# Performance work log

Measured on AMD Instinct MI355X. Metric: run time of the kernel, lower is better.

The kernel has to match this reference:

```python
import jax, jax.numpy as jnp
import numpy as np

D_MODEL = 1024
N_HEADS = 16
D_HEAD = D_MODEL // N_HEADS
BLOCK = 2048
EPS = 1e-5


def layer_norm(x, w, b):
    mu = jnp.mean(x, axis=-1, keepdims=True)
    var = jnp.mean(jnp.square(x - mu), axis=-1, keepdims=True)
    return (x - mu) * jax.lax.rsqrt(var + EPS) * w + b


def setup_inputs() -> dict:
    key = jax.random.key(0)
    ks = jax.random.split(key, 8)
    d = D_MODEL
    s = 1.0 / np.sqrt(d)
    return {
        "x": jax.random.normal(ks[0], (2, 2048, d), dtype=jnp.float32),
        "ln1_w": jnp.ones((d,), jnp.float32),
        "ln1_b": jnp.zeros((d,), jnp.float32),
        "ln2_w": jnp.ones((d,), jnp.float32),
        "ln2_b": jnp.zeros((d,), jnp.float32),
        "qkv_w": jax.random.normal(ks[1], (3 * d, d), jnp.float32) * s,
        "o_w": jax.random.normal(ks[2], (d, d), jnp.float32) * s,
        "ffn_w1": jax.random.normal(ks[3], (4 * d, d), jnp.float32) * s,
        "ffn_b1": jnp.zeros((4 * d,), jnp.float32),
        "ffn_w2": jax.random.normal(ks[4], (d, 4 * d), jnp.float32) * (1.0 / np.sqrt(4 * d)),
        "ffn_b2": jnp.zeros((d,), jnp.float32),
    }


def reference(x, ln1_w, ln1_b, ln2_w, ln2_b, qkv_w, o_w, ffn_w1, ffn_b1, ffn_w2, ffn_b2):
    b, n, d = x.shape
    h = layer_norm(x, ln1_w, ln1_b)
    # qkv: (b, n, 3, H, Dh)
    qkv = (h @ qkv_w.T).reshape(b, n, 3, N_HEADS, D_HEAD)
    q, k, v = qkv[:, :, 0], qkv[:, :, 1], qkv[:, :, 2]  # (b, n, H, Dh)
    scale = 1.0 / np.sqrt(D_HEAD)
    s = jnp.einsum("bqhd,bkhd->bhqk", q, k) * scale
    mask = jnp.tril(jnp.ones((n, n), dtype=bool))
    s = jnp.where(mask, s, -jnp.inf)
    a = jax.nn.softmax(s, axis=-1)
    attn_out = jnp.einsum("bhqk,bkhd->bqhd", a, v).reshape(b, n, d)
    x = x + attn_out @ o_w.T
    h2 = layer_norm(x, ln2_w, ln2_b)
    ff = jax.nn.gelu(h2 @ ffn_w1.T + ffn_b1, approximate=False) @ ffn_w2.T + ffn_b2
    return x + ff
```

## Files before the change

kernel.cpp:

```cpp
#include <hip/hip_runtime.h>
#include <math.h>

#define D_MODEL 1024
#define N_HEADS 16
#define D_HEAD  64
#define SEQ     2048
#define BATCH   2
#define M_TOT   (BATCH*SEQ)
#define FFN_DIM 4096

typedef __attribute__((ext_vector_type(8))) short bf16x8;
typedef __attribute__((ext_vector_type(4))) float f32x4;
typedef __attribute__((ext_vector_type(8))) unsigned short u16x8;

__device__ __forceinline__ unsigned short f2bf(float f) {
  unsigned int u = __float_as_uint(f);
  return (unsigned short)((u + 0x7fffu + ((u >> 16) & 1u)) >> 16);
}
__device__ __forceinline__ unsigned short f2bf_trunc(float f) {
  return (unsigned short)(__float_as_uint(f) >> 16);
}
__device__ __forceinline__ float bf2f(unsigned short s) {
  return __uint_as_float(((unsigned int)s) << 16);
}

__device__ __forceinline__ float gelu_exact(float x) {
  return 0.5f * x * (1.f + erff(x * 0.70710678118654752f));
}

__global__ __launch_bounds__(256) void cvt_all(const float* __restrict__ qkv_w,
    const float* __restrict__ o_w, const float* __restrict__ w1,
    const float* __restrict__ w2, unsigned short* __restrict__ dst) {
  const long MEGc = 1024*1024;
  long i = (long)(blockIdx.x*256 + threadIdx.x)*4;
  const float* src; long off;
  if (i < 3*MEGc)      { src = qkv_w; off = i; }
  else if (i < 4*MEGc) { src = o_w;  off = i - 3*MEGc; }
  else if (i < 8*MEGc) { src = w1;   off = i - 4*MEGc; }
  else                 { src = w2;   off = i - 8*MEGc; }
  float4 v = *(const float4*)(src + off);
  ushort4 o = { f2bf(v.x), f2bf(v.y), f2bf(v.z), f2bf(v.w) };
  *(ushort4*)(dst + i) = o;
}

__global__ __launch_bounds__(256) void ln_kernel(const float* __restrict__ x,
    const float* __restrict__ w, const float* __restrict__ b,
    unsigned short* __restrict__ out) {
  int row = blockIdx.x;
  const float* xr = x + (size_t)row * D_MODEL;
  int c = threadIdx.x * 4;
  float4 v = *(const float4*)(xr + c);
  float s = v.x + v.y + v.z + v.w;
  __shared__ float red[4];
  #pragma unroll
  for (int o = 32; o > 0; o >>= 1) s += __shfl_down(s, o, 64);
  int wave = threadIdx.x >> 6;
  if ((threadIdx.x & 63) == 0) red[wave] = s;
  __syncthreads();
  float mean = (red[0]+red[1]+red[2]+red[3]) * (1.f/D_MODEL);
  __syncthreads();
  float d0 = v.x-mean, d1 = v.y-mean, d2 = v.z-mean, d3 = v.w-mean;
  float s2 = d0*d0 + d1*d1 + d2*d2 + d3*d3;
  #pragma unroll
  for (int o = 32; o > 0; o >>= 1) s2 += __shfl_down(s2, o, 64);
  if ((threadIdx.x & 63) == 0) red[wave] = s2;
  __syncthreads();
  float var = (red[0]+red[1]+red[2]+red[3]) * (1.f/D_MODEL);
  float rs = rsqrtf(var + 1e-5f);
  float4 wv = *(const float4*)(w + c);
  float4 bv = *(const float4*)(b + c);
  ushort4 o = { f2bf(d0*rs*wv.x + bv.x), f2bf(d1*rs*wv.y + bv.y),
                f2bf(d2*rs*wv.z + bv.z), f2bf(d3*rs*wv.w + bv.w) };
  *(ushort4*)(out + (size_t)row*D_MODEL + c) = o;
}

__device__ __forceinline__ void swizzle_block(int nbx, int nby, int& bx, int& by) {
  int nb = nbx * nby;
  int bid = blockIdx.y * nbx + blockIdx.x;
  int chunk = nb >> 3;
  int bid2 = (bid & 7) * chunk + (bid >> 3);
  const int GM = 8;
  int ngroup = GM * nbx;
  int g = bid2 / ngroup, rem = bid2 % ngroup;
  by = g*GM + (rem % GM);
  bx = rem / GM;
}

template<int EPI, bool OBF, int BN>
__global__ __launch_bounds__(256) void gemm_mfma(
    const unsigned short* __restrict__ A, const unsigned short* __restrict__ Bt,
    float* __restrict__ Cf, unsigned short* __restrict__ Cb,
    const float* __restrict__ bias, const float* __restrict__ res,
    int M, int N, int K) {
  constexpr int BM = 128, BK = 32;
  constexpr int TS = (BM + BN) * BK;
  constexpr int CPT = TS / 2048;
  constexpr int NI = (BN == 128) ? 4 : 2;
  __shared__ unsigned short Ls[2][TS];
  int tid = threadIdx.x;
  int w = tid >> 6, l = tid & 63;
  int lg = l >> 4, lm = l & 15;
  int bx, by;
  swizzle_block(N/BN, M/BM, bx, by);
  int bm = by * BM, bn = bx * BN;
  int wm = (w >> 1) * 64;
  int wn = (w & 1) * (BN/2);

  f32x4 acc[4][NI];
  #pragma unroll
  for (int i = 0; i < 4; ++i)
    #pragma unroll
    for (int j = 0; j < NI; ++j)
      acc[i][j] = (f32x4){0.f, 0.f, 0.f, 0.f};

  const unsigned short* gp[CPT];
  int lo[CPT];
  #pragma unroll
  for (int i = 0; i < CPT; ++i) {
    int fc = i*256 + tid;
    int r = fc >> 2;
    int swz = (fc >> 3) & 3;
    int col = ((fc & 3) ^ swz) * 8;
    lo[i] = fc * 8;
    gp[i] = (r < BM) ? (A  + (size_t)(bm + r)*K + col)
                     : (Bt + (size_t)(bn + (r - BM))*K + col);
  }
  u16x8 sreg[CPT];
  auto loadregs = [&](int k0) {
    #pragma unroll
    for (int i = 0; i < CPT; ++i) sreg[i] = *(const u16x8*)(gp[i] + k0);
  };
  auto dswrite = [&](int buf) {
    #pragma unroll
    for (int i = 0; i < CPT; ++i) *(u16x8*)&Ls[buf][lo[i]] = sreg[i];
  };

  int lgs = lg ^ ((lm >> 1) & 3);
  int aoff = (wm + lm)*BK + lgs*8;
  int boff = BM*BK + (wn + lm)*BK + lgs*8;

  auto compute = [&](int buf) {
    bf16x8 af[4], bfr[NI];
    #pragma unroll
    for (int i = 0; i < 4; ++i)  af[i]  = *(const bf16x8*)&Ls[buf][aoff + i*512];
    #pragma unroll
    for (int j = 0; j < NI; ++j) bfr[j] = *(const bf16x8*)&Ls[buf][boff + j*512];
    #pragma unroll
    for (int i = 0; i < 4; ++i)
      #pragma unroll
      for (int j = 0; j < NI; ++j)
        acc[i][j] = __builtin_amdgcn_mfma_f32_16x16x32_bf16(af[i], bfr[j], acc[i][j], 0, 0, 0);
  };

  loadregs(0);
  dswrite(0);
  __syncthreads();
  int niter = K / BK;
  for (int kt = 0; kt < niter; ++kt) {
    if (kt + 1 < niter) loadregs((kt+1)*BK);
    compute(kt & 1);
    if (kt + 1 < niter) {
      dswrite((kt+1) & 1);
      __syncthreads();
    }
  }

  #pragma unroll
  for (int i = 0; i < 4; ++i) {
    #pragma unroll
    for (int j = 0; j < NI; ++j) {
      int col = bn + wn + j*16 + lm;
      #pragma unroll
      for (int r = 0; r < 4; ++r) {
        int row = bm + wm + i*16 + lg*4 + r;
        float v = acc[i][j][r];
        if (EPI == 1) v = gelu_exact(v + bias[col]);
        if (EPI == 2) v += res[(size_t)row*N + col];
        if (EPI == 3) v += bias[col] + res[(size_t)row*N + col];
        if (OBF) Cb[(size_t)row*N + col] = f2bf(v);
        else     Cf[(size_t)row*N + col] = v;
      }
    }
  }
}

__global__ __launch_bounds__(256) void vtrans_kernel(
    const unsigned short* __restrict__ qkvb, unsigned short* __restrict__ vT) {
  __shared__ unsigned short T[64*72];
  int nt = blockIdx.x, h = blockIdx.y, b = blockIdx.z;
  int tid = threadIdx.x;
  const unsigned short* vb = qkvb + (size_t)(b*SEQ)*(3*D_MODEL) + 2*D_MODEL + h*D_HEAD;
  #pragma unroll
  for (int it = 0; it < 2; ++it) {
    int idx = tid + it*256;
    int r = idx >> 3, c8 = (idx & 7)*8;
    *(u16x8*)&T[r*72 + c8] = *(const u16x8*)(vb + (size_t)(nt*64 + r)*(3*D_MODEL) + c8);
  }
  __syncthreads();
  unsigned short* vto = vT + ((size_t)(b*N_HEADS + h)*D_HEAD)*SEQ + nt*64;
  #pragma unroll
  for (int it = 0; it < 2; ++it) {
    int idx = tid + it*256;
    int d = idx >> 3, s8 = (idx & 7)*8;
    u16x8 o;
    #pragma unroll
    for (int i = 0; i < 8; ++i) o[i] = T[(s8+i)*72 + d];
    *(u16x8*)(vto + (size_t)d*SEQ + s8) = o;
  }
}

#define ATT_PAD 72
__device__ __forceinline__ void attn_step(
    const bf16x8* aq, float* m_i, float* l_i, f32x4* acc_o,
    const unsigned short* __restrict__ Ks, const unsigned short* __restrict__ Vt,
    unsigned short* __restrict__ pw, int lg, int lm, int qoff, bool diag) {
  f32x4 sacc[4];
  #pragma unroll
  for (int j = 0; j < 4; ++j) sacc[j] = (f32x4){0.f, 0.f, 0.f, 0.f};
  #pragma unroll
  for (int s = 0; s < 2; ++s)
    #pragma unroll
    for (int j = 0; j < 4; ++j)
      sacc[j] = __builtin_amdgcn_mfma_f32_16x16x32_bf16(
          aq[s], *(const bf16x8*)&Ks[(j*16+lm)*ATT_PAD + s*32 + lg*8], sacc[j], 0, 0, 0);
  if (diag) {
    #pragma unroll
    for (int j = 0; j < 4; ++j)
      #pragma unroll
      for (int r = 0; r < 4; ++r)
        if (j*16 + lm > qoff + lg*4 + r) sacc[j][r] = -INFINITY;
  }
  float alpha[4];
  #pragma unroll
  for (int r = 0; r < 4; ++r) {
    float rm = fmaxf(fmaxf(sacc[0][r], sacc[1][r]), fmaxf(sacc[2][r], sacc[3][r]));
    #pragma unroll
    for (int o = 1; o < 16; o <<= 1) rm = fmaxf(rm, __shfl_xor(rm, o));
    float mn = fmaxf(m_i[r], rm);
    alpha[r] = __expf(m_i[r] - mn);
    float rsum = 0.f;
    #pragma unroll
    for (int j = 0; j < 4; ++j) {
      float p = __expf(sacc[j][r] - mn);
      sacc[j][r] = p; rsum += p;
    }
    #pragma unroll
    for (int o = 1; o < 16; o <<= 1) rsum += __shfl_xor(rsum, o);
    l_i[r] = l_i[r]*alpha[r] + rsum;
    m_i[r] = mn;
  }
  #pragma unroll
  for (int j = 0; j < 4; ++j)
    #pragma unroll
    for (int r = 0; r < 4; ++r)
      pw[(lg*4 + r)*ATT_PAD + j*16 + lm] = f2bf_trunc(sacc[j][r]);
  #pragma unroll
  for (int j = 0; j < 4; ++j)
    #pragma unroll
    for (int r = 0; r < 4; ++r)
      acc_o[j][r] *= alpha[r];
  #pragma unroll
  for (int s = 0; s < 2; ++s) {
    bf16x8 ap = *(const bf16x8*)&pw[lm*ATT_PAD + s*32 + lg*8];
    #pragma unroll
    for (int j = 0; j < 4; ++j)
      acc_o[j] = __builtin_amdgcn_mfma_f32_16x16x32_bf16(
          ap, *(const bf16x8*)&Vt[(j*16+lm)*ATT_PAD + s*32 + lg*8], acc_o[j], 0, 0, 0);
  }
}

__global__ __launch_bounds__(256) void attn_mfma_kernel(
    const unsigned short* __restrict__ qkvb, const unsigned short* __restrict__ vT,
    unsigned short* __restrict__ out) {
  __shared__ unsigned short Ks[64*ATT_PAD];
  __shared__ unsigned short Vt[64*ATT_PAD];
  __shared__ unsigned short Pw[4][16*ATT_PAD];

  int pr = blockIdx.x, h = blockIdx.y, b = blockIdx.z;
  int qtH = 31 - pr, qtL = pr;
  int tid = threadIdx.x;
  int w = tid >> 6, l = tid & 63;
  int lg = l >> 4, lm = l & 15;

  const size_t rs3 = 3*D_MODEL;
  const unsigned short* qb  = qkvb + (size_t)(b*SEQ)*rs3 + h*D_HEAD;
  const unsigned short* kb  = qb + D_MODEL;
  const unsigned short* vtb = vT + ((size_t)(b*N_HEADS + h)*D_HEAD)*SEQ;

  bf16x8 aqH[2], aqL[2];
  int qrH = qtH*64 + w*16 + lm, qrL = qtL*64 + w*16 + lm;
  #pragma unroll
  for (int s = 0; s < 2; ++s) {
    u16x8 tH = *(const u16x8*)(qb + (size_t)qrH*rs3 + s*32 + lg*8);
    u16x8 tL = *(const u16x8*)(qb + (size_t)qrL*rs3 + s*32 + lg*8);
    bf16x8 rH, rL;
    #pragma unroll
    for (int i = 0; i < 8; ++i) {
      rH[i] = (short)f2bf(bf2f(tH[i]) * 0.125f);
      rL[i] = (short)f2bf(bf2f(tL[i]) * 0.125f);
    }
    aqH[s] = rH; aqL[s] = rL;
  }

  float mH[4], lH[4], mL[4], lL[4];
  f32x4 oH[4], oL[4];
  #pragma unroll
  for (int r = 0; r < 4; ++r) { mH[r] = -INFINITY; lH[r] = 0.f; mL[r] = -INFINITY; lL[r] = 0.f; }
  #pragma unroll
  for (int j = 0; j < 4; ++j) { oH[j] = (f32x4){0.f,0.f,0.f,0.f}; oL[j] = (f32x4){0.f,0.f,0.f,0.f}; }

  unsigned short* pw = &Pw[w][0];

  int sidx0 = tid, sidx1 = tid + 256;
  int sr0 = sidx0 >> 3, sc0 = (sidx0 & 7)*8;
  int sr1 = sidx1 >> 3, sc1 = (sidx1 & 7)*8;

  u16x8 kreg[2], vreg[2];
  auto prefetch = [&](int kt) {
    kreg[0] = *(const u16x8*)(kb  + (size_t)(kt*64 + sr0)*rs3 + sc0);
    kreg[1] = *(const u16x8*)(kb  + (size_t)(kt*64 + sr1)*rs3 + sc1);
    vreg[0] = *(const u16x8*)(vtb + (size_t)sr0*SEQ + kt*64 + sc0);
    vreg[1] = *(const u16x8*)(vtb + (size_t)sr1*SEQ + kt*64 + sc1);
  };

  prefetch(0);
  for (int kt = 0; kt <= qtH; ++kt) {
    __syncthreads();
    *(u16x8*)&Ks[sr0*ATT_PAD + sc0] = kreg[0];
    *(u16x8*)&Ks[sr1*ATT_PAD + sc1] = kreg[1];
    *(u16x8*)&Vt[sr0*ATT_PAD + sc0] = vreg[0];
    *(u16x8*)&Vt[sr1*ATT_PAD + sc1] = vreg[1];
    __syncthreads();
    if (kt < qtH) prefetch(kt+1);
    attn_step(aqH, mH, lH, oH, Ks, Vt, pw, lg, lm, w*16, kt == qtH);
    if (kt <= qtL)
      attn_step(aqL, mL, lL, oL, Ks, Vt, pw, lg, lm, w*16, kt == qtL);
  }

  #pragma unroll
  for (int r = 0; r < 4; ++r) {
    float invH = 1.f / lH[r], invL = 1.f / lL[r];
    int qH = qtH*64 + w*16 + lg*4 + r;
    int qL = qtL*64 + w*16 + lg*4 + r;
    #pragma unroll
    for (int j = 0; j < 4; ++j) {
      out[((size_t)(b*SEQ + qH))*D_MODEL + h*D_HEAD + j*16 + lm] = f2bf(oH[j][r]*invH);
      out[((size_t)(b*SEQ + qL))*D_MODEL + h*D_HEAD + j*16 + lm] = f2bf(oL[j][r]*invL);
    }
  }
}

extern "C" void kernel_launch(void* const* d_in, const int* in_sizes, int n_in,
                              void* d_out, int out_size, void* d_ws, size_t ws_size,
                              hipStream_t stream) {
  const float* x      = (const float*)d_in[0];
  const float* ln1_w  = (const float*)d_in[1];
  const float* ln1_b  = (const float*)d_in[2];
  const float* ln2_w  = (const float*)d_in[3];
  const float* ln2_b  = (const float*)d_in[4];
  const float* qkv_w  = (const float*)d_in[5];
  const float* o_w    = (const float*)d_in[6];
  const float* ffn_w1 = (const float*)d_in[7];
  const float* ffn_b1 = (const float*)d_in[8];
  const float* ffn_w2 = (const float*)d_in[9];
  const float* ffn_b2 = (const float*)d_in[10];
  float* out = (float*)d_out;
  float* ws  = (float*)d_ws;

  const size_t MEG = 1024*1024;
  unsigned short* wqkv = (unsigned short*)ws;
  unsigned short* wo   = wqkv + 3*MEG;
  unsigned short* w1   = wo   + 1*MEG;
  unsigned short* w2   = w1   + 4*MEG;
  unsigned short* hbf    = (unsigned short*)(ws + 6*MEG);
  unsigned short* attnbf = (unsigned short*)(ws + 8*MEG);
  float* x1  = ws + 10*MEG;
  unsigned short* qkvb = (unsigned short*)(ws + 14*MEG);
  unsigned short* ffbf = (unsigned short*)(ws + 14*MEG);
  unsigned short* vT   = (unsigned short*)(ws + 22*MEG);

  cvt_all<<<12*MEG/1024, 256, 0, stream>>>(qkv_w, o_w, ffn_w1, ffn_w2, wqkv);
  ln_kernel<<<M_TOT, 256, 0, stream>>>(x, ln1_w, ln1_b, hbf);
  gemm_mfma<0,true,128><<<dim3(3*D_MODEL/128, M_TOT/128), 256, 0, stream>>>(
      hbf, wqkv, nullptr, qkvb, nullptr, nullptr, M_TOT, 3*D_MODEL, D_MODEL);
  vtrans_kernel<<<dim3(SEQ/64, N_HEADS, BATCH), 256, 0, stream>>>(qkvb, vT);
  attn_mfma_kernel<<<dim3(16, N_HEADS, BATCH), 256, 0, stream>>>(qkvb, vT, attnbf);
  gemm_mfma<2,false,64><<<dim3(D_MODEL/64, M_TOT/128), 256, 0, stream>>>(
      attnbf, wo, x1, nullptr, nullptr, x, M_TOT, D_MODEL, D_MODEL);
  ln_kernel<<<M_TOT, 256, 0, stream>>>(x1, ln2_w, ln2_b, hbf);
  gemm_mfma<1,true,128><<<dim3(FFN_DIM/128, M_TOT/128), 256, 0, stream>>>(
      hbf, w1, nullptr, ffbf, ffn_b1, nullptr, M_TOT, FFN_DIM, D_MODEL);
  gemm_mfma<3,false,64><<<dim3(D_MODEL/64, M_TOT/128), 256, 0, stream>>>(
      ffbf, w2, out, nullptr, ffn_b2, x1, M_TOT, D_MODEL, FFN_DIM);
}
```

Measured before the change: 375.4 us.

## Add 256x256-tile GEMM with direct global-to-LDS loads for QKV and FFN1

Adds a new GEMM kernel with 256x256 output tiles, 512 threads, BK=64, XOR-swizzled LDS layout and double-buffered global_load_lds staging, and uses it for the QKV projection and the first FFN layer. Larger tiles raise arithmetic intensity and cut global traffic per FLOP, and the direct-to-LDS loads bypass register staging. The risks are fewer blocks (e.g. 192 for QKV) relative to the CU count, which can hurt occupancy and wave balance, and scalar bf16 stores in the epilogue that may be poorly coalesced.

```diff
diff --git a/kernel.cpp b/kernel.cpp
--- a/kernel.cpp
+++ b/kernel.cpp
@@ -27,6 +27,16 @@
 __device__ __forceinline__ float gelu_exact(float x) {
   return 0.5f * x * (1.f + erff(x * 0.70710678118654752f));
 }
+
+__device__ __forceinline__ void block_sync() {
+  asm volatile("" ::: "memory");
+  __builtin_amdgcn_s_barrier();
+  asm volatile("" ::: "memory");
+}
+
+#define GLL16(g, l) __builtin_amdgcn_global_load_lds( \
+    (const __attribute__((address_space(1))) unsigned int*)(g), \
+    (__attribute__((address_space(3))) unsigned int*)(l), 16, 0, 0)
 
 __global__ __launch_bounds__(256) void cvt_all(const float* __restrict__ qkv_w,
     const float* __restrict__ o_w, const float* __restrict__ w1,
@@ -84,6 +94,120 @@
   int g = bid2 / ngroup, rem = bid2 % ngroup;
   by = g*GM + (rem % GM);
   bx = rem / GM;
+}
+
+template<int EPI>
+__global__ __launch_bounds__(512, 2) void gemm256(
+    const unsigned short* __restrict__ A, const unsigned short* __restrict__ Bt,
+    unsigned short* __restrict__ Cb, const float* __restrict__ bias,
+    int M, int N, int K) {
+  __shared__ unsigned short As[2][256*64];
+  __shared__ unsigned short Bs[2][256*64];
+  int tid = threadIdx.x;
+  int l = tid & 63;
+  int w = tid >> 6;
+  int lg = l >> 4, lm = l & 15;
+  int wr = w >> 2, wc = w & 3;
+  int bx, by;
+  swizzle_block(N/256, M/256, bx, by);
+  int bm = by * 256, bn = bx * 256;
+
+  const unsigned short* gA[4];
+  const unsigned short* gB[4];
+  #pragma unroll
+  for (int i = 0; i < 4; ++i) {
+    int f = i*512 + tid;
+    int r = f >> 3;
+    int qg = (f & 7) ^ (r & 7);
+    gA[i] = A  + (size_t)(bm + r)*K + qg*8;
+    gB[i] = Bt + (size_t)(bn + r)*K + qg*8;
+  }
+  auto stage = [&](int buf, int k0) {
+    #pragma unroll
+    for (int i = 0; i < 4; ++i)
+      GLL16(gA[i] + k0, &As[buf][(i*512 + tid)*8]);
+    #pragma unroll
+    for (int i = 0; i < 4; ++i)
+      GLL16(gB[i] + k0, &Bs[buf][(i*512 + tid)*8]);
+  };
+
+  stage(0, 0);
+  stage(1, 64);
+
+  f32x4 acc[8][4];
+  #pragma unroll
+  for (int i = 0; i < 8; ++i)
+    #pragma unroll
+    for (int j = 0; j < 4; ++j)
+      acc[i][j] = (f32x4){0.f, 0.f, 0.f, 0.f};
+
+  asm volatile("s_waitcnt vmcnt(8)" ::: "memory");
+  block_sync();
+
+  int nt = K >> 6;
+  for (int t = 0; t < nt; ++t) {
+    const unsigned short* as = As[t & 1];
+    const unsigned short* bs = Bs[t & 1];
+    bf16x8 bfr[4][2];
+    #pragma unroll
+    for (int j = 0; j < 4; ++j) {
+      int rb = wc*64 + j*16 + lm;
+      #pragma unroll
+      for (int ks = 0; ks < 2; ++ks)
+        bfr[j][ks] = *(const bf16x8*)&bs[rb*64 + ((ks*4 + lg) ^ (rb & 7))*8];
+    }
+    #pragma unroll
+    for (int p = 0; p < 4; ++p) {
+      bf16x8 af[2][2];
+      #pragma unroll
+      for (int i = 0; i < 2; ++i) {
+        int ra = wr*128 + (p*2 + i)*16 + lm;
+        #pragma unroll
+        for (int ks = 0; ks < 2; ++ks)
+          af[i][ks] = *(const bf16x8*)&as[ra*64 + ((ks*4 + lg) ^ (ra & 7))*8];
+      }
+      __builtin_amdgcn_s_setprio(1);
+      #pragma unroll
+      for (int i = 0; i < 2; ++i)
+        #pragma unroll
+        for (int j = 0; j < 4; ++j)
+          #pragma unroll
+          for (int ks = 0; ks < 2; ++ks)
+            acc[p*2+i][j] = __builtin_amdgcn_mfma_f32_16x16x32_bf16(
+                af[i][ks], bfr[j][ks], acc[p*2+i][j], 0, 0, 0);
+      __builtin_amdgcn_s_setprio(0);
+    }
+    if (t + 1 < nt) {
+      block_sync();
+      if (t + 2 < nt) {
+        stage(t & 1, (t + 2) << 6);
+        asm volatile("s_waitcnt vmcnt(8)" ::: "memory");
+      } else {
+        asm volatile("s_waitcnt vmcnt(0)" ::: "memory");
+      }
+      block_sync();
+    }
+  }
+
+  float bv[4];
+  if (EPI == 1) {
+    #pragma unroll
+    for (int j = 0; j < 4; ++j) bv[j] = bias[bn + wc*64 + j*16 + lm];
+  }
+  #pragma unroll
+  for (int i = 0; i < 8; ++i) {
+    #pragma unroll
+    for (int j = 0; j < 4; ++j) {
+      int col = bn + wc*64 + j*16 + lm;
+      #pragma unroll
+      for (int r = 0; r < 4; ++r) {
+        int row = bm + wr*128 + i*16 + lg*4 + r;
+        float v = acc[i][j][r];
+        if (EPI == 1) v = gelu_exact(v + bv[j]);
+        Cb[(size_t)row*N + col] = f2bf(v);
+      }
+    }
+  }
 }
 
 template<int EPI, bool OBF, int BN>
@@ -381,15 +505,15 @@
 
   cvt_all<<<12*MEG/1024, 256, 0, stream>>>(qkv_w, o_w, ffn_w1, ffn_w2, wqkv);
   ln_kernel<<<M_TOT, 256, 0, stream>>>(x, ln1_w, ln1_b, hbf);
-  gemm_mfma<0,true,128><<<dim3(3*D_MODEL/128, M_TOT/128), 256, 0, stream>>>(
-      hbf, wqkv, nullptr, qkvb, nullptr, nullptr, M_TOT, 3*D_MODEL, D_MODEL);
+  gemm256<0><<<dim3(3*D_MODEL/256, M_TOT/256), 512, 0, stream>>>(
+      hbf, wqkv, qkvb, nullptr, M_TOT, 3*D_MODEL, D_MODEL);
   vtrans_kernel<<<dim3(SEQ/64, N_HEADS, BATCH), 256, 0, stream>>>(qkvb, vT);
   attn_mfma_kernel<<<dim3(16, N_HEADS, BATCH), 256, 0, stream>>>(qkvb, vT, attnbf);
   gemm_mfma<2,false,64><<<dim3(D_MODEL/64, M_TOT/128), 256, 0, stream>>>(
       attnbf, wo, x1, nullptr, nullptr, x, M_TOT, D_MODEL, D_MODEL);
   ln_kernel<<<M_TOT, 256, 0, stream>>>(x1, ln2_w, ln2_b, hbf);
-  gemm_mfma<1,true,128><<<dim3(FFN_DIM/128, M_TOT/128), 256, 0, stream>>>(
-      hbf, w1, nullptr, ffbf, ffn_b1, nullptr, M_TOT, FFN_DIM, D_MODEL);
+  gemm256<1><<<dim3(FFN_DIM/256, M_TOT/256), 512, 0, stream>>>(
+      hbf, w1, ffbf, ffn_b1, M_TOT, FFN_DIM, D_MODEL);
   gemm_mfma<3,false,64><<<dim3(D_MODEL/64, M_TOT/128), 256, 0, stream>>>(
       ffbf, w2, out, nullptr, ffn_b2, x1, M_TOT, D_MODEL, FFN_DIM);
 }
```

Result: slower. 437.4 us (+16.5%).
